# Optimization experiments

Measured on AMD Instinct MI355X. Metric: run time of the kernel, lower is better.

The kernel has to match this reference:

```python
import jax, jax.numpy as jnp
import numpy as np

L = 4        # num_layers
B = 32       # batch
N = 512      # num_nodes == seq_len
D = 256      # d_model
H = 8        # nhead
HD = D // H  # head_dim
F = 1024     # dim_feedforward
EPS = 1e-5


def setup_inputs() -> dict:
    key = jax.random.key(0)
    ks = jax.random.split(key, 12)
    w = lambda k, shape: jax.random.normal(k, shape, jnp.float32) * 0.02
    return {
        "src": jax.random.normal(ks[0], (B, N, D), jnp.float32),
        # node embeddings (torch.randn -> std 1)
        "e1": jax.random.normal(ks[1], (N, D), jnp.float32),
        "e2": jax.random.normal(ks[2], (N, D), jnp.float32),
        # per-layer attention projections, stored [L, d_in, d_out]
        "Wq": w(ks[3], (L, D, D)), "bq": jnp.zeros((L, D), jnp.float32),
        "Wk": w(ks[4], (L, D, D)), "bk": jnp.zeros((L, D), jnp.float32),
        "Wv": w(ks[5], (L, D, D)), "bv": jnp.zeros((L, D), jnp.float32),
        "Wo": w(ks[6], (L, D, D)), "bo": jnp.zeros((L, D), jnp.float32),
        # FFN
        "W1": w(ks[7], (L, D, F)), "b1": jnp.zeros((L, F), jnp.float32),
        "W2": w(ks[8], (L, F, D)), "b2": jnp.zeros((L, D), jnp.float32),
        # LayerNorms
        "g1": jnp.ones((L, D), jnp.float32), "be1": jnp.zeros((L, D), jnp.float32),
        "g2": jnp.ones((L, D), jnp.float32), "be2": jnp.zeros((L, D), jnp.float32),
    }


def _layernorm(x, g, b):
    mu = jnp.mean(x, axis=-1, keepdims=True)
    var = jnp.mean(jnp.square(x - mu), axis=-1, keepdims=True)
    return (x - mu) * jax.lax.rsqrt(var + EPS) * g + b


def reference(src, e1, e2, Wq, bq, Wk, bk, Wv, bv, Wo, bo,
              W1, b1, W2, b2, g1, be1, g2, be2):
    # adaptive spatial bias shared across all layers: [N, N]
    bias = jnp.matmul(e1, e2.T)
    scale = 1.0 / jnp.sqrt(jnp.float32(HD))
    x = src
    for l in range(L):
        def heads(t):  # [B,N,D] -> [B,H,N,HD]
            return t.reshape(B, N, H, HD).transpose(0, 2, 1, 3)
        q = heads(x @ Wq[l] + bq[l])
        k = heads(x @ Wk[l] + bk[l])
        v = heads(x @ Wv[l] + bv[l])
        # scores + shared additive bias (broadcast over batch and heads)
        scores = jnp.einsum('bhqd,bhkd->bhqk', q, k) * scale + bias
        attn = jax.nn.softmax(scores, axis=-1)
        o = jnp.einsum('bhqk,bhkd->bhqd', attn, v)
        o = o.transpose(0, 2, 1, 3).reshape(B, N, D) @ Wo[l] + bo[l]
        x = _layernorm(x + o, g1[l], be1[l])
        ff = jax.nn.relu(x @ W1[l] + b1[l]) @ W2[l] + b2[l]
        x = _layernorm(x + ff, g2[l], be2[l])
    return x
```

## Files before the change

kernel.cpp:

```cpp
#include <hip/hip_runtime.h>

typedef __bf16 bf16;
typedef __bf16 v4bf __attribute__((ext_vector_type(4)));
typedef __bf16 v8bf __attribute__((ext_vector_type(8)));
typedef float  v4f  __attribute__((ext_vector_type(4)));
typedef float  v16f __attribute__((ext_vector_type(16)));
typedef unsigned short u16;
typedef u16 v8us __attribute__((ext_vector_type(8)));
typedef unsigned int v4u __attribute__((ext_vector_type(4)));

#define L_ 4
#define B_ 32
#define N_ 512
#define D_ 256
#define H_ 8
#define F_ 1024
#define ROWS (B_*N_)
#define QHSZ ((size_t)B_*H_*N_*32)

__device__ __forceinline__ void gload16(const void* g, void* l) {
  __builtin_amdgcn_global_load_lds((__attribute__((address_space(1))) void*)g,
                                   (__attribute__((address_space(3))) void*)l,
                                   16, 0, 0);
}

__device__ __forceinline__ unsigned pk_bf16(float a, float b) {
  unsigned r;
  asm("v_cvt_pk_bf16_f32 %0, %1, %2" : "=v"(r) : "v"(a), "v"(b));
  return r;
}

#define PLSWAP(a, b) asm volatile("v_permlane32_swap_b32 %0, %1" : "+v"(a), "+v"(b))

#define EXP2(x) __builtin_amdgcn_exp2f(x)

template <int N> __device__ __forceinline__ void waitvm() {
  if constexpr (N == 0) asm volatile("s_waitcnt vmcnt(0)" ::: "memory");
  else if constexpr (N == 2) asm volatile("s_waitcnt vmcnt(2)" ::: "memory");
  else if constexpr (N == 3) asm volatile("s_waitcnt vmcnt(3)" ::: "memory");
  else if constexpr (N == 4) asm volatile("s_waitcnt vmcnt(4)" ::: "memory");
  else if constexpr (N == 5) asm volatile("s_waitcnt vmcnt(5)" ::: "memory");
  else if constexpr (N == 6) asm volatile("s_waitcnt vmcnt(6)" ::: "memory");
}

__global__ __launch_bounds__(256) void bias_gemm(
    const float* __restrict__ e1, const float* __restrict__ e2,
    float* __restrict__ biasP) {
  __shared__ float As[16][16];
  __shared__ float Bs[16][16];
  const int tx = threadIdx.x, ty = threadIdx.y;
  const int r = blockIdx.y * 16 + ty, c = blockIdx.x * 16 + tx;
  float acc = 0.f;
  for (int k0 = 0; k0 < D_; k0 += 16) {
    As[ty][tx] = e1[r * D_ + k0 + tx];
    Bs[ty][tx] = e2[(blockIdx.x * 16 + ty) * D_ + k0 + tx];
    __syncthreads();
#pragma unroll
    for (int kk = 0; kk < 16; ++kk) acc += As[ty][kk] * Bs[tx][kk];
    __syncthreads();
  }
  const int kb = r >> 5, r5 = r & 31;
  const int blk = kb * 8 + (r5 >> 3) * 2 + ((r5 >> 2) & 1);
  biasP[(size_t)(blk * 512 + c) * 4 + (r5 & 3)] = acc * 1.4426950408889634f;
}

__global__ __launch_bounds__(256) void colmax(
    const float* __restrict__ biasP, float* __restrict__ mq) {
  const int q = blockIdx.x * 256 + threadIdx.x;
  float mx = -1e30f;
  for (int blk = 0; blk < 128; ++blk) {
    const float4 v = *(const float4*)&biasP[(size_t)(blk * 512 + q) * 4];
    mx = fmaxf(mx, fmaxf(fmaxf(v.x, v.y), fmaxf(v.z, v.w)));
  }
  mq[q] = mx;
}

__global__ __launch_bounds__(256) void subm(
    float* __restrict__ biasP, const float* __restrict__ mq) {
  const int i = blockIdx.x * 256 + threadIdx.x;
  float4 v = ((float4*)biasP)[i];
  const float m = mq[i & 511];
  v.x -= m; v.y -= m; v.z -= m; v.w -= m;
  ((float4*)biasP)[i] = v;
}

__device__ __forceinline__ void convT_tile(
    const float* __restrict__ W, bf16* __restrict__ Wt,
    int K, int N, size_t inL, size_t outL, int l, int k0, int n0, int tid,
    float (*t)[33]) {
  const int r = tid >> 5, c = tid & 31;
#pragma unroll
  for (int i = 0; i < 4; ++i)
    t[r + 8 * i][c] = W[l * inL + (size_t)(k0 + r + 8 * i) * N + n0 + c];
  __syncthreads();
#pragma unroll
  for (int i = 0; i < 4; ++i)
    Wt[l * outL + (size_t)(n0 + r + 8 * i) * K + k0 + c] = (bf16)t[c][r + 8 * i];
}

__global__ __launch_bounds__(256) void setup_all(
    const float* __restrict__ src, bf16* __restrict__ xb,
    const float* __restrict__ bq, const float* __restrict__ bk,
    const float* __restrict__ bv, float* __restrict__ bqkv,
    const float* __restrict__ Wq, const float* __restrict__ Wk,
    const float* __restrict__ Wv, const float* __restrict__ Wo,
    const float* __restrict__ W1, const float* __restrict__ W2,
    bf16* __restrict__ Wqkvt, bf16* __restrict__ Wot,
    bf16* __restrict__ W1t, bf16* __restrict__ W2t) {
  __shared__ float t[32][33];
  const int tid = threadIdx.x;
  int id = blockIdx.x;
  if (id < 4096) {
    const int i = id * 256 + tid;
    float4 v = ((const float4*)src)[i];
    uint2 w;
    w.x = pk_bf16(v.x, v.y);
    w.y = pk_bf16(v.z, v.w);
    ((uint2*)xb)[i] = w;
    return;
  }
  id -= 4096;
  if (id < 12) {
    const int i = id * 256 + tid;
    if (i < L_ * 768) {
      const int l = i / 768, n = i - l * 768;
      float v = (n < 256) ? bq[l * 256 + n]
              : (n < 512) ? bk[l * 256 + n - 256]
                          : bv[l * 256 + n - 512];
      bqkv[i] = v;
    }
    return;
  }
  id -= 12;
  if (id < 1024) {
    const int w = id >> 8, tt = id & 255;
    const int l = tt >> 6, tile = tt & 63;
    const int n0 = (tile & 7) * 32, k0 = (tile >> 3) * 32;
    const float* W = (w == 0) ? Wq : (w == 1) ? Wk : (w == 2) ? Wv : Wo;
    bf16* Wt = (w == 3) ? Wot : (Wqkvt + w * 65536);
    const size_t outL = (w == 3) ? 65536 : 196608;
    convT_tile(W, Wt, 256, 256, 65536, outL, l, k0, n0, tid, t);
    return;
  }
  id -= 1024;
  if (id < 1024) {
    const int l = id >> 8, tile = id & 255;
    const int n0 = (tile & 31) * 32, k0 = (tile >> 5) * 32;
    convT_tile(W1, W1t, 256, 1024, 262144, 262144, l, k0, n0, tid, t);
    return;
  }
  id -= 1024;
  {
    const int l = id >> 8, tile = id & 255;
    const int n0 = (tile & 7) * 32, k0 = (tile >> 3) * 32;
    convT_tile(W2, W2t, 1024, 256, 262144, 262144, l, k0, n0, tid, t);
  }
}

template <int BM, int BN, int WPC, int RELU, int OUTMODE, int RESID>
__global__ __launch_bounds__(256, WPC) void gemm_bf16k(
    const bf16* __restrict__ A, const bf16* __restrict__ Bt,
    const float* __restrict__ bias, const bf16* __restrict__ resid,
    void* __restrict__ Cout, int M, int N, int K, int nbx) {
  constexpr int MR = BM / 32, NR = BN / 32;
  constexpr int NSLAB = (BM + BN) / 16;
  constexpr int LPW = NSLAB / 4;
  constexpr int BUFE = (BM + BN) * 32;
  __shared__ __align__(16) bf16 lds[3 * BUFE];
  const int tid  = threadIdx.x;
  const int wave = tid >> 6, lane = tid & 63;
  const int l15 = lane & 15, l4 = lane >> 4;
  const int qq = gridDim.x >> 3;
  const int wg = (blockIdx.x & 7) * qq + (blockIdx.x >> 3);
  const int bx = wg % nbx, by = wg / nbx;
  const int bm = by * BM, bn = bx * BN;
  const int wr = (wave >> 1) * (BM / 2), wc = (wave & 1) * (BN / 2);
  const int lrow = lane >> 2;
  const int lk   = (lane & 3) * 8;

  v4f acc[MR][NR];
#pragma unroll
  for (int m = 0; m < MR; ++m)
#pragma unroll
    for (int n = 0; n < NR; ++n) acc[m][n] = (v4f){0.f, 0.f, 0.f, 0.f};

  auto STAGE = [&](int buf, int k0) {
    bf16* dst = &lds[buf * BUFE];
#pragma unroll
    for (int s = wave; s < NSLAB; s += 4) {
      if (s < BM / 16)
        gload16(A + (size_t)(bm + s * 16 + lrow) * K + k0 + lk, dst + s * 512);
      else
        gload16(Bt + (size_t)(bn + (s - BM / 16) * 16 + lrow) * K + k0 + lk, dst + s * 512);
    }
  };

  const int nk = K >> 5;
  STAGE(0, 0);
  STAGE(1, 32);
  waitvm<LPW>();
  __builtin_amdgcn_s_barrier();
  __builtin_amdgcn_sched_barrier(0);

  int cur = 0;
  for (int t = 0; t < nk; ++t) {
    const bool pf = (t + 2 < nk);
    if (pf) STAGE(cur == 0 ? 2 : cur - 1, (t + 2) * 32);
    const bf16* buf = &lds[cur * BUFE];
    v8bf af[MR], bfr[NR];
#pragma unroll
    for (int m = 0; m < MR; ++m)
      af[m] = *(const v8bf*)&buf[(wr + m * 16 + l15) * 32 + l4 * 8];
#pragma unroll
    for (int n = 0; n < NR; ++n)
      bfr[n] = *(const v8bf*)&buf[BM * 32 + (wc + n * 16 + l15) * 32 + l4 * 8];
    __builtin_amdgcn_s_setprio(1);
#pragma unroll
    for (int m = 0; m < MR; ++m)
#pragma unroll
      for (int n = 0; n < NR; ++n)
        acc[m][n] = __builtin_amdgcn_mfma_f32_16x16x32_bf16(af[m], bfr[n], acc[m][n], 0, 0, 0);
    __builtin_amdgcn_s_setprio(0);
    if (pf) waitvm<LPW>();
    else    waitvm<0>();
    __builtin_amdgcn_s_barrier();
    __builtin_amdgcn_sched_barrier(0);
    cur = (cur == 2) ? 0 : cur + 1;
  }

#pragma unroll
  for (int m = 0; m < MR; ++m) {
    const int row0 = bm + wr + m * 16 + l4 * 4;
#pragma unroll
    for (int n = 0; n < NR; ++n) {
      const int col = bn + wc + n * 16 + l15;
      const float bc = bias[col];
      if constexpr (OUTMODE == 2) {
        const int sec = col >> 8, hh = (col >> 5) & 7, d = col & 31;
        const int bb = row0 >> 9, nr0 = row0 & 511;
        bf16* dst = (bf16*)Cout + (size_t)sec * QHSZ +
                    (((size_t)bb * 8 + hh) * 512 + nr0) * 32 + d;
#pragma unroll
        for (int i = 0; i < 4; ++i)
          dst[i * 32] = (bf16)(acc[m][n][i] + bc);
      } else {
#pragma unroll
        for (int i = 0; i < 4; ++i) {
          const size_t idx = (size_t)(row0 + i) * N + col;
          float v = acc[m][n][i] + bc;
          if (RESID) v += (float)resid[idx];
          if (RELU) v = fmaxf(v, 0.f);
          if (OUTMODE == 1) ((bf16*)Cout)[idx] = (bf16)v;
          else              ((float*)Cout)[idx] = v;
        }
      }
    }
  }
}

#define VTS 520
__global__ __launch_bounds__(256, 3) void attn_k(
    const bf16* __restrict__ qkvh, const float* __restrict__ biasP,
    bf16* __restrict__ outp) {
  __shared__ u16 Vt[32 * VTS];
  const int tid = threadIdx.x;
  const int wave = tid >> 6, lane = tid & 63;
  const int l31 = lane & 31, hi = lane >> 5;
  const int fid = blockIdx.x;
  const int xcd = fid & 7, idx = fid >> 3;
  const int b = (xcd << 2) | (idx >> 5);
  const int h = (idx & 31) >> 2;
  const int qblk = idx & 3;
  const u16* Qh = (const u16*)qkvh + (((size_t)b * 8 + h) * 512) * 32;
  const u16* Kh = Qh + QHSZ;
  const u16* Vh = Qh + 2 * QHSZ;
  const int qb = qblk * 128 + wave * 32;

  {
    const u16* p0 = Vh + (size_t)(2 * tid) * 32;
    const u16* p1 = p0 + 32;
#pragma unroll
    for (int d0 = 0; d0 < 32; d0 += 8) {
      v8us a = *(const v8us*)(p0 + d0);
      v8us c = *(const v8us*)(p1 + d0);
#pragma unroll
      for (int j = 0; j < 8; ++j) {
        unsigned u = (unsigned)a[j] | ((unsigned)c[j] << 16);
        *(unsigned*)&Vt[(d0 + j) * VTS + tid * 2] = u;
      }
    }
  }
  __syncthreads();

  const u16* qrow = Qh + (size_t)(qb + l31) * 32;
  const v8bf qf0 = *(const v8bf*)(qrow + hi * 8);
  const v8bf qf1 = *(const v8bf*)(qrow + 16 + hi * 8);
  const float* bpl = biasP + ((size_t)(hi * 512 + qb + l31)) * 4;

  const float SC2 = 0.17677669529663688f * 1.4426950408889634f;
  float lsum = 0.f;
  v16f accO = {0.f,0.f,0.f,0.f,0.f,0.f,0.f,0.f,0.f,0.f,0.f,0.f,0.f,0.f,0.f,0.f};

  v8bf ka0 = *(const v8bf*)(Kh + (size_t)l31 * 32 + hi * 8);
  v8bf ka1 = *(const v8bf*)(Kh + (size_t)l31 * 32 + 16 + hi * 8);
  v4f bb[4];
#pragma unroll
  for (int g = 0; g < 4; ++g) bb[g] = *(const v4f*)(bpl + (size_t)(g * 2) * 2048);

  v16f stC = {0.f,0.f,0.f,0.f,0.f,0.f,0.f,0.f,0.f,0.f,0.f,0.f,0.f,0.f,0.f,0.f};
  stC = __builtin_amdgcn_mfma_f32_32x32x16_bf16(ka0, qf0, stC, 0, 0, 0);
  stC = __builtin_amdgcn_mfma_f32_32x32x16_bf16(ka1, qf1, stC, 0, 0, 0);
  {
    const u16* kn = Kh + (size_t)(32 + l31) * 32;
    ka0 = *(const v8bf*)(kn + hi * 8);
    ka1 = *(const v8bf*)(kn + 16 + hi * 8);
  }

  for (int kb = 0; kb < 16; ++kb) {
    const int kbase = kb * 32;
    v16f stN = {0.f,0.f,0.f,0.f,0.f,0.f,0.f,0.f,0.f,0.f,0.f,0.f,0.f,0.f,0.f,0.f};
    __builtin_amdgcn_s_setprio(1);
    stN = __builtin_amdgcn_mfma_f32_32x32x16_bf16(ka0, qf0, stN, 0, 0, 0);
    stN = __builtin_amdgcn_mfma_f32_32x32x16_bf16(ka1, qf1, stN, 0, 0, 0);
    __builtin_amdgcn_s_setprio(0);

    const u16* kn = Kh + (size_t)(kbase + 64 + l31) * 32;
    const v8bf kn0 = *(const v8bf*)(kn + hi * 8);
    const v8bf kn1 = *(const v8bf*)(kn + 16 + hi * 8);
    v4f bn[4];
#pragma unroll
    for (int g = 0; g < 4; ++g)
      bn[g] = *(const v4f*)(bpl + (size_t)((kb + 1) * 8 + g * 2) * 2048);

    float p[16];
#pragma unroll
    for (int r = 0; r < 16; ++r)
      p[r] = EXP2(stC[r] * SC2 + bb[r >> 2][r & 3]);

    float s8[8], s4[4];
#pragma unroll
    for (int r = 0; r < 8; ++r) s8[r] = p[r] + p[r + 8];
#pragma unroll
    for (int r = 0; r < 4; ++r) s4[r] = s8[r] + s8[r + 4];
    lsum += (s4[0] + s4[2]) + (s4[1] + s4[3]);

    unsigned u[8];
#pragma unroll
    for (int t = 0; t < 8; ++t) u[t] = pk_bf16(p[2 * t], p[2 * t + 1]);
    PLSWAP(u[0], u[2]);
    PLSWAP(u[1], u[3]);
    PLSWAP(u[4], u[6]);
    PLSWAP(u[5], u[7]);
    union { v4u u; v8bf h; } cv0, cv1;
    cv0.u = (v4u){u[0], u[1], u[2], u[3]};
    cv1.u = (v4u){u[4], u[5], u[6], u[7]};

    const v8bf va0 = *(const v8bf*)&Vt[l31 * VTS + kbase + hi * 8];
    const v8bf va1 = *(const v8bf*)&Vt[l31 * VTS + kbase + 16 + hi * 8];
    __builtin_amdgcn_s_setprio(1);
    accO = __builtin_amdgcn_mfma_f32_32x32x16_bf16(va0, cv0.h, accO, 0, 0, 0);
    accO = __builtin_amdgcn_mfma_f32_32x32x16_bf16(va1, cv1.h, accO, 0, 0, 0);
    __builtin_amdgcn_s_setprio(0);

    stC = stN;
    ka0 = kn0; ka1 = kn1;
#pragma unroll
    for (int g = 0; g < 4; ++g) bb[g] = bn[g];
  }

  lsum += __shfl_xor(lsum, 32);

  const float inv = 1.0f / lsum;
  u16* orow = (u16*)outp + (size_t)(b * N_ + qb + l31) * D_ + h * 32 + 4 * hi;
#pragma unroll
  for (int g = 0; g < 4; ++g) {
    uint2 w;
    w.x = pk_bf16(accO[4 * g] * inv, accO[4 * g + 1] * inv);
    w.y = pk_bf16(accO[4 * g + 2] * inv, accO[4 * g + 3] * inv);
    *(uint2*)(orow + 8 * g) = w;
  }
}

template <int MODE>
__global__ __launch_bounds__(256) void ln_kernel(
    const float* __restrict__ xin,
    const float* __restrict__ g, const float* __restrict__ b,
    float* __restrict__ xout_f32, bf16* __restrict__ xbout) {
  const int wv = threadIdx.x >> 6, ln = threadIdx.x & 63;
  const size_t row = blockIdx.x * 4 + wv;
  const size_t o4 = row * D_ + ln * 4;
  const float4 v = *(const float4*)&xin[o4];
  float s  = (v.x + v.y) + (v.z + v.w);
  float ss = (v.x * v.x + v.y * v.y) + (v.z * v.z + v.w * v.w);
#pragma unroll
  for (int off = 1; off < 64; off <<= 1) {
    s  += __shfl_xor(s, off);
    ss += __shfl_xor(ss, off);
  }
  const float mu = s * (1.f / D_);
  const float var = ss * (1.f / D_) - mu * mu;
  const float rs = rsqrtf(var + 1e-5f);
  const float4 gg = *(const float4*)&g[ln * 4];
  const float4 bb = *(const float4*)&b[ln * 4];
  float4 o;
  o.x = (v.x - mu) * rs * gg.x + bb.x;
  o.y = (v.y - mu) * rs * gg.y + bb.y;
  o.z = (v.z - mu) * rs * gg.z + bb.z;
  o.w = (v.w - mu) * rs * gg.w + bb.w;
  if constexpr (MODE == 1) {
    *(float4*)&xout_f32[o4] = o;
  } else {
    uint2 w;
    w.x = pk_bf16(o.x, o.y);
    w.y = pk_bf16(o.z, o.w);
    *(uint2*)&xbout[o4] = w;
  }
}

extern "C" void kernel_launch(void* const* d_in, const int* in_sizes, int n_in,
                              void* d_out, int out_size, void* d_ws, size_t ws_size,
                              hipStream_t stream) {
  const float* src = (const float*)d_in[0];
  const float* e1  = (const float*)d_in[1];
  const float* e2  = (const float*)d_in[2];
  const float* Wq  = (const float*)d_in[3];
  const float* bq  = (const float*)d_in[4];
  const float* Wk  = (const float*)d_in[5];
  const float* bk  = (const float*)d_in[6];
  const float* Wv  = (const float*)d_in[7];
  const float* bv  = (const float*)d_in[8];
  const float* Wo  = (const float*)d_in[9];
  const float* bo  = (const float*)d_in[10];
  const float* W1  = (const float*)d_in[11];
  const float* b1  = (const float*)d_in[12];
  const float* W2  = (const float*)d_in[13];
  const float* b2  = (const float*)d_in[14];
  const float* g1  = (const float*)d_in[15];
  const float* be1 = (const float*)d_in[16];
  const float* g2  = (const float*)d_in[17];
  const float* be2 = (const float*)d_in[18];

  char* ws = (char*)d_ws;
  size_t off = 0;
  auto alloc = [&](size_t bytes) {
    void* p = ws + off;
    off += (bytes + 255) & ~(size_t)255;
    return p;
  };
  float* biasP  = (float*)alloc((size_t)2 * 1024 * 1024);
  float* mq     = (float*)alloc((size_t)N_ * 4);
  bf16*  xb     = (bf16*) alloc((size_t)ROWS * D_ * 2);
  bf16*  attn_o = (bf16*) alloc((size_t)ROWS * D_ * 2);
  float* tmpf   = (float*)alloc((size_t)ROWS * D_ * 4);
  bf16*  qkvh   = (bf16*) alloc((size_t)ROWS * 1024 * 2 + 65536);
  bf16*  h1     = qkvh;
  bf16*  Wqkvt  = (bf16*) alloc((size_t)L_ * 768 * 256 * 2);
  bf16*  Wot    = (bf16*) alloc((size_t)L_ * 256 * 256 * 2);
  bf16*  W1t    = (bf16*) alloc((size_t)L_ * 1024 * 256 * 2);
  bf16*  W2t    = (bf16*) alloc((size_t)L_ * 256 * 1024 * 2);
  float* bqkv   = (float*)alloc((size_t)L_ * 768 * 4);

  bias_gemm<<<dim3(32, 32), dim3(16, 16), 0, stream>>>(e2, e1, biasP);
  colmax<<<2, 256, 0, stream>>>(biasP, mq);
  subm<<<256, 256, 0, stream>>>(biasP, mq);
  setup_all<<<7180, 256, 0, stream>>>(
      src, xb, bq, bk, bv, bqkv,
      Wq, Wk, Wv, Wo, W1, W2, Wqkvt, Wot, W1t, W2t);

  for (int l = 0; l < L_; ++l) {
    gemm_bf16k<128, 128, 3, 0, 2, 0><<<768, 256, 0, stream>>>(
        xb, Wqkvt + (size_t)l * 196608, bqkv + l * 768, nullptr, qkvh,
        ROWS, 768, 256, 6);
    attn_k<<<1024, 256, 0, stream>>>(qkvh, biasP, attn_o);
    gemm_bf16k<64, 128, 4, 0, 0, 1><<<512, 256, 0, stream>>>(
        attn_o, Wot + (size_t)l * 65536, bo + l * 256, xb, tmpf,
        ROWS, 256, 256, 2);
    ln_kernel<0><<<ROWS / 4, 256, 0, stream>>>(tmpf, g1 + l * 256, be1 + l * 256, nullptr, xb);
    gemm_bf16k<128, 128, 3, 1, 1, 0><<<1024, 256, 0, stream>>>(
        xb, W1t + (size_t)l * 262144, b1 + l * 1024, nullptr, h1,
        ROWS, 1024, 256, 8);
    gemm_bf16k<64, 128, 4, 0, 0, 1><<<512, 256, 0, stream>>>(
        h1, W2t + (size_t)l * 262144, b2 + l * 256, xb, tmpf,
        ROWS, 256, 1024, 2);
    if (l == L_ - 1)
      ln_kernel<1><<<ROWS / 4, 256, 0, stream>>>(tmpf, g2 + l * 256, be2 + l * 256, (float*)d_out, nullptr);
    else
      ln_kernel<0><<<ROWS / 4, 256, 0, stream>>>(tmpf, g2 + l * 256, be2 + l * 256, nullptr, xb);
  }
}
```

Measured before the change: 475.6 us.

## Fuse bias column-max into bias GEMM, enlarge attention blocks and FFN1 tiles

```diff
diff --git a/kernel.cpp b/kernel.cpp
--- a/kernel.cpp
+++ b/kernel.cpp
@@ -34,6 +34,15 @@
 
 #define EXP2(x) __builtin_amdgcn_exp2f(x)
 
+__device__ __forceinline__ unsigned encf(float f) {
+  unsigned u = __float_as_uint(f);
+  return (u & 0x80000000u) ? ~u : (u | 0x80000000u);
+}
+__device__ __forceinline__ float decf(unsigned e) {
+  unsigned b = (e & 0x80000000u) ? (e & 0x7fffffffu) : ~e;
+  return __uint_as_float(b);
+}
+
 template <int N> __device__ __forceinline__ void waitvm() {
   if constexpr (N == 0) asm volatile("s_waitcnt vmcnt(0)" ::: "memory");
   else if constexpr (N == 2) asm volatile("s_waitcnt vmcnt(2)" ::: "memory");
@@ -45,7 +54,7 @@
 
 __global__ __launch_bounds__(256) void bias_gemm(
     const float* __restrict__ e1, const float* __restrict__ e2,
-    float* __restrict__ biasP) {
+    float* __restrict__ biasP, unsigned* __restrict__ mqe) {
   __shared__ float As[16][16];
   __shared__ float Bs[16][16];
   const int tx = threadIdx.x, ty = threadIdx.y;
@@ -59,27 +68,25 @@
     for (int kk = 0; kk < 16; ++kk) acc += As[ty][kk] * Bs[tx][kk];
     __syncthreads();
   }
+  acc *= 1.4426950408889634f;
   const int kb = r >> 5, r5 = r & 31;
   const int blk = kb * 8 + (r5 >> 3) * 2 + ((r5 >> 2) & 1);
-  biasP[(size_t)(blk * 512 + c) * 4 + (r5 & 3)] = acc * 1.4426950408889634f;
-}
-
-__global__ __launch_bounds__(256) void colmax(
-    const float* __restrict__ biasP, float* __restrict__ mq) {
-  const int q = blockIdx.x * 256 + threadIdx.x;
-  float mx = -1e30f;
-  for (int blk = 0; blk < 128; ++blk) {
-    const float4 v = *(const float4*)&biasP[(size_t)(blk * 512 + q) * 4];
-    mx = fmaxf(mx, fmaxf(fmaxf(v.x, v.y), fmaxf(v.z, v.w)));
-  }
-  mq[q] = mx;
+  biasP[(size_t)(blk * 512 + c) * 4 + (r5 & 3)] = acc;
+  As[ty][tx] = acc;
+  __syncthreads();
+  if (ty == 0) {
+    float m = As[0][tx];
+#pragma unroll
+    for (int j = 1; j < 16; ++j) m = fmaxf(m, As[j][tx]);
+    atomicMax(&mqe[c], encf(m));
+  }
 }
 
 __global__ __launch_bounds__(256) void subm(
-    float* __restrict__ biasP, const float* __restrict__ mq) {
+    float* __restrict__ biasP, const unsigned* __restrict__ mqe) {
   const int i = blockIdx.x * 256 + threadIdx.x;
   float4 v = ((float4*)biasP)[i];
-  const float m = mq[i & 511];
+  const float m = decf(mqe[i & 511]);
   v.x -= m; v.y -= m; v.z -= m; v.w -= m;
   ((float4*)biasP)[i] = v;
 }
@@ -259,7 +266,7 @@
 }
 
 #define VTS 520
-__global__ __launch_bounds__(256, 3) void attn_k(
+__global__ __launch_bounds__(512, 2) void attn_k(
     const bf16* __restrict__ qkvh, const float* __restrict__ biasP,
     bf16* __restrict__ outp) {
   __shared__ u16 Vt[32 * VTS];
@@ -268,26 +275,22 @@
   const int l31 = lane & 31, hi = lane >> 5;
   const int fid = blockIdx.x;
   const int xcd = fid & 7, idx = fid >> 3;
-  const int b = (xcd << 2) | (idx >> 5);
-  const int h = (idx & 31) >> 2;
-  const int qblk = idx & 3;
+  const int b = (xcd << 2) | (idx >> 4);
+  const int h = (idx >> 1) & 7;
+  const int qhalf = idx & 1;
   const u16* Qh = (const u16*)qkvh + (((size_t)b * 8 + h) * 512) * 32;
   const u16* Kh = Qh + QHSZ;
   const u16* Vh = Qh + 2 * QHSZ;
-  const int qb = qblk * 128 + wave * 32;
+  const int qb = qhalf * 256 + wave * 32;
 
   {
-    const u16* p0 = Vh + (size_t)(2 * tid) * 32;
-    const u16* p1 = p0 + 32;
+    const u16* p0 = Vh + (size_t)tid * 32;
 #pragma unroll
     for (int d0 = 0; d0 < 32; d0 += 8) {
       v8us a = *(const v8us*)(p0 + d0);
-      v8us c = *(const v8us*)(p1 + d0);
-#pragma unroll
-      for (int j = 0; j < 8; ++j) {
-        unsigned u = (unsigned)a[j] | ((unsigned)c[j] << 16);
-        *(unsigned*)&Vt[(d0 + j) * VTS + tid * 2] = u;
-      }
+#pragma unroll
+      for (int j = 0; j < 8; ++j)
+        Vt[(d0 + j) * VTS + tid] = a[j];
     }
   }
   __syncthreads();
@@ -447,22 +450,22 @@
     off += (bytes + 255) & ~(size_t)255;
     return p;
   };
-  float* biasP  = (float*)alloc((size_t)2 * 1024 * 1024);
-  float* mq     = (float*)alloc((size_t)N_ * 4);
-  bf16*  xb     = (bf16*) alloc((size_t)ROWS * D_ * 2);
-  bf16*  attn_o = (bf16*) alloc((size_t)ROWS * D_ * 2);
-  float* tmpf   = (float*)alloc((size_t)ROWS * D_ * 4);
-  bf16*  qkvh   = (bf16*) alloc((size_t)ROWS * 1024 * 2 + 65536);
-  bf16*  h1     = qkvh;
-  bf16*  Wqkvt  = (bf16*) alloc((size_t)L_ * 768 * 256 * 2);
-  bf16*  Wot    = (bf16*) alloc((size_t)L_ * 256 * 256 * 2);
-  bf16*  W1t    = (bf16*) alloc((size_t)L_ * 1024 * 256 * 2);
-  bf16*  W2t    = (bf16*) alloc((size_t)L_ * 256 * 1024 * 2);
-  float* bqkv   = (float*)alloc((size_t)L_ * 768 * 4);
-
-  bias_gemm<<<dim3(32, 32), dim3(16, 16), 0, stream>>>(e2, e1, biasP);
-  colmax<<<2, 256, 0, stream>>>(biasP, mq);
-  subm<<<256, 256, 0, stream>>>(biasP, mq);
+  float*    biasP  = (float*)alloc((size_t)2 * 1024 * 1024);
+  unsigned* mqe    = (unsigned*)alloc((size_t)N_ * 4);
+  bf16*     xb     = (bf16*) alloc((size_t)ROWS * D_ * 2);
+  bf16*     attn_o = (bf16*) alloc((size_t)ROWS * D_ * 2);
+  float*    tmpf   = (float*)alloc((size_t)ROWS * D_ * 4);
+  bf16*     qkvh   = (bf16*) alloc((size_t)ROWS * 1024 * 2 + 65536);
+  bf16*     h1     = qkvh;
+  bf16*     Wqkvt  = (bf16*) alloc((size_t)L_ * 768 * 256 * 2);
+  bf16*     Wot    = (bf16*) alloc((size_t)L_ * 256 * 256 * 2);
+  bf16*     W1t    = (bf16*) alloc((size_t)L_ * 1024 * 256 * 2);
+  bf16*     W2t    = (bf16*) alloc((size_t)L_ * 256 * 1024 * 2);
+  float*    bqkv   = (float*)alloc((size_t)L_ * 768 * 4);
+
+  hipMemsetAsync(mqe, 0, (size_t)N_ * 4, stream);
+  bias_gemm<<<dim3(32, 32), dim3(16, 16), 0, stream>>>(e2, e1, biasP, mqe);
+  subm<<<256, 256, 0, stream>>>(biasP, mqe);
   setup_all<<<7180, 256, 0, stream>>>(
       src, xb, bq, bk, bv, bqkv,
       Wq, Wk, Wv, Wo, W1, W2, Wqkvt, Wot, W1t, W2t);
@@ -471,14 +474,14 @@
     gemm_bf16k<128, 128, 3, 0, 2, 0><<<768, 256, 0, stream>>>(
         xb, Wqkvt + (size_t)l * 196608, bqkv + l * 768, nullptr, qkvh,
         ROWS, 768, 256, 6);
-    attn_k<<<1024, 256, 0, stream>>>(qkvh, biasP, attn_o);
+    attn_k<<<512, 512, 0, stream>>>(qkvh, biasP, attn_o);
     gemm_bf16k<64, 128, 4, 0, 0, 1><<<512, 256, 0, stream>>>(
         attn_o, Wot + (size_t)l * 65536, bo + l * 256, xb, tmpf,
         ROWS, 256, 256, 2);
     ln_kernel<0><<<ROWS / 4, 256, 0, stream>>>(tmpf, g1 + l * 256, be1 + l * 256, nullptr, xb);
-    gemm_bf16k<128, 128, 3, 1, 1, 0><<<1024, 256, 0, stream>>>(
+    gemm_bf16k<128, 256, 2, 1, 1, 0><<<512, 256, 0, stream>>>(
         xb, W1t + (size_t)l * 262144, b1 + l * 1024, nullptr, h1,
-        ROWS, 1024, 256, 8);
+        ROWS, 1024, 256, 4);
     gemm_bf16k<64, 128, 4, 0, 0, 1><<<512, 256, 0, stream>>>(
         h1, W2t + (size_t)l * 262144, b2 + l * 256, xb, tmpf,
         ROWS, 256, 1024, 2);
```

Result: faster. 452.3 us (-4.9%).
